# Kernel optimization log

Hardware: AMD Instinct MI355X
Metric: run time of the kernel (lower is better)

The kernel has to match this reference:

```python
import jax, jax.numpy as jnp
import numpy as np

M_BITS = 8   # mantissa bits (m in BlockQuantize)
E_BITS = 8   # exponent bits (e)
GROUP_D = 64 # column-group width from group_shapes [64,64]


def bfp_quantize_2d(W, d=GROUP_D, m=M_BITS, e=E_BITS):
    """Faithful vectorized BlockQuantize2D with calculate_bias=True.
    Groups = 64-wide column blocks spanning all rows (tensor.reshape(-1,d)[start::new_width])."""
    a, b = W.shape
    nw = b // d
    # [nw, a*d]: each row is one quantization group
    blocks = W.reshape(a, nw, d).transpose(1, 0, 2).reshape(nw, a * d)
    maxv = jnp.max(jnp.abs(blocks), axis=1, keepdims=True)
    bias = 2.0 ** e - jnp.log2(maxv) + jnp.log2(2.0 - 2.0 ** (-m + 1)) - 1.0
    max_exp = 2.0 ** e - 1.0 - bias
    max_val = 2.0 ** max_exp * (1.0 + (1.0 - 2.0 ** (-m - 1)))
    sign = jnp.sign(blocks)
    absx = jnp.clip(jnp.abs(blocks), -max_val, max_val)  # lower bound negative -> no-op, as in source
    exponent = jnp.floor(jnp.log2(absx + 1e-40))
    mantissa = absx / 2.0 ** exponent                    # in [1, 2)
    group_exp = jnp.max(exponent, axis=1, keepdims=True)
    group_exp = jnp.where(group_exp + bias < 1.0, -bias, group_exp)
    # shiftTruncateInBinaryForm
    factor = 2 ** (m - 1)                                # 128
    sm = (mantissa * factor).astype(jnp.int32)           # [128, 256)
    shift = jnp.clip((group_exp - exponent).astype(jnp.int32), 0, 31)
    shifted = jnp.right_shift(sm, shift)
    safe = jnp.maximum(shifted, 1)
    bitlen = (jnp.floor(jnp.log2(safe.astype(jnp.float32))) + 1.0).astype(jnp.int32)
    mask = jnp.where(bitlen > 8, jnp.left_shift(jnp.int32(255), bitlen - 8), jnp.int32(255))
    trunc = jnp.bitwise_and(shifted, mask).astype(jnp.float32) / factor
    q = sign * trunc * 2.0 ** group_exp
    return q.reshape(nw, a, d).transpose(1, 0, 2).reshape(a, b)


def apply_rope(t, cos, sin):
    """t: [b,s,h,hd]; complex rotation on (even, odd) pairs as in apply_rotary_emb."""
    tr = t.reshape(*t.shape[:-1], -1, 2)
    te, to = tr[..., 0], tr[..., 1]
    c = cos[None, :, None, :]
    s = sin[None, :, None, :]
    oe = te * c - to * s
    oo = te * s + to * c
    return jnp.stack([oe, oo], axis=-1).reshape(t.shape)


def setup_inputs() -> dict:
    key = jax.random.key(0)
    k = jax.random.split(key, 5)
    dim, n_heads, n_kv, hd = 4096, 32, 8, 128
    b, s = 1, 2048
    x = jax.random.normal(k[0], (b, s, dim), jnp.float32)
    wq = jax.random.normal(k[1], (n_heads * hd, dim), jnp.float32) * 0.02
    wk = jax.random.normal(k[2], (n_kv * hd, dim), jnp.float32) * 0.02
    wv = jax.random.normal(k[3], (n_kv * hd, dim), jnp.float32) * 0.02
    wo = jax.random.normal(k[4], (dim, n_heads * hd), jnp.float32) * 0.02
    inv_freq = 1.0 / (10000.0 ** (jnp.arange(0, hd, 2, dtype=jnp.float32) / hd))
    ang = jnp.outer(jnp.arange(s, dtype=jnp.float32), inv_freq)  # [s, hd/2]
    return {"x": x, "wq": wq, "wk": wk, "wv": wv, "wo": wo,
            "freqs_cos": jnp.cos(ang), "freqs_sin": jnp.sin(ang)}


def reference(x, wq, wk, wv, wo, freqs_cos, freqs_sin):
    b, s, dim = x.shape
    n_heads, n_kv, hd = 32, 8, 128
    n_rep = n_heads // n_kv
    # block-floating-point quantization of projection weights (per-64-column groups)
    wq_q = bfp_quantize_2d(wq)
    wk_q = bfp_quantize_2d(wk)
    wv_q = bfp_quantize_2d(wv)
    wo_q = bfp_quantize_2d(wo)
    q = jnp.einsum('bsd,od->bso', x, wq_q).reshape(b, s, n_heads, hd)
    kk = jnp.einsum('bsd,od->bso', x, wk_q).reshape(b, s, n_kv, hd)
    v = jnp.einsum('bsd,od->bso', x, wv_q).reshape(b, s, n_kv, hd)
    q = apply_rope(q, freqs_cos, freqs_sin)
    kk = apply_rope(kk, freqs_cos, freqs_sin)
    # repeat_kv: GQA expand kv heads by n_rep
    kk = jnp.repeat(kk, n_rep, axis=2)  # [b,s,n_heads,hd]
    v = jnp.repeat(v, n_rep, axis=2)
    scores = jnp.einsum('bshd,bthd->bhst', q, kk) / jnp.sqrt(jnp.float32(hd))
    causal = jnp.triu(jnp.full((s, s), -jnp.inf, dtype=scores.dtype), k=1)
    probs = jax.nn.softmax(scores + causal, axis=-1)
    out = jnp.einsum('bhst,bthd->bshd', probs, v).reshape(b, s, n_heads * hd)
    return jnp.einsum('bso,do->bsd', out, wo_q)
```

## Files before the change

### kernel.cpp

```cpp
#include <hip/hip_runtime.h>
#include <hip/hip_bf16.h>

typedef __hip_bfloat16 hbf16;
typedef __bf16 bf16x8 __attribute__((ext_vector_type(8)));
typedef float f32x4 __attribute__((ext_vector_type(4)));

#define MFMA16(a, b, c) __builtin_amdgcn_mfma_f32_16x16x32_bf16((a), (b), (c), 0, 0, 0)

#define ASYNC16(ldsaddr, gaddr)                                                        \
  __builtin_amdgcn_global_load_lds(                                                    \
      (__attribute__((address_space(1))) void*)(void*)(gaddr),                         \
      (__attribute__((address_space(3))) void*)(ldsaddr), 16, 0, 0)

static __device__ __forceinline__ float fexp2(float x) {
#if __has_builtin(__builtin_amdgcn_exp2f)
  return __builtin_amdgcn_exp2f(x);
#else
  return exp2f(x);
#endif
}

__global__ void init_gmax_kernel(unsigned int* g) { g[threadIdx.x] = 0u; }

__global__ void quant_max_kernel(const float* __restrict__ wq, const float* __restrict__ wk,
                                 const float* __restrict__ wv, const float* __restrict__ wo,
                                 unsigned int* __restrict__ gmax) {
  const int my = blockIdx.y;
  const float* W;
  int slotBase, rowsPerSplit;
  if (my == 0) { W = wq; slotBase = 0;   rowsPerSplit = 512; }
  else if (my == 1) { W = wk; slotBase = 64;  rowsPerSplit = 128; }
  else if (my == 2) { W = wv; slotBase = 128; rowsPerSplit = 128; }
  else { W = wo; slotBase = 192; rowsPerSplit = 512; }
  const int tid = threadIdx.x;
  const int group = blockIdx.x & 63;
  const int split = blockIdx.x >> 6;
  const int c4 = (tid & 15) * 4;
  const int rs = tid >> 4;
  const float* base = W + (size_t)(split * rowsPerSplit) * 4096 + group * 64 + c4;
  float m = 0.f;
  for (int r = rs; r < rowsPerSplit; r += 16) {
    float4 v = *(const float4*)(base + (size_t)r * 4096);
    m = fmaxf(m, fmaxf(fmaxf(fabsf(v.x), fabsf(v.y)), fmaxf(fabsf(v.z), fabsf(v.w))));
  }
  for (int d = 1; d < 64; d <<= 1) m = fmaxf(m, __shfl_xor(m, d, 64));
  __shared__ float wm_[4];
  if ((tid & 63) == 0) wm_[tid >> 6] = m;
  __syncthreads();
  if (tid == 0) {
    m = fmaxf(fmaxf(wm_[0], wm_[1]), fmaxf(wm_[2], wm_[3]));
    atomicMax(gmax + slotBase + group, __float_as_uint(m));
  }
}

__device__ __forceinline__ void quant_body(const float* __restrict__ W, hbf16* __restrict__ Wq,
                                           const unsigned int* __restrict__ gmax, int slotBase,
                                           int n4) {
  const int stride = gridDim.x * 256;
  for (int idx = blockIdx.x * 256 + threadIdx.x; idx < n4; idx += stride) {
    int group = (idx & 1023) >> 4;
    unsigned int mb = gmax[slotBase + group];
    int gex = (int)((mb >> 23) & 255) - 127;
    float s = __uint_as_float((unsigned)(134 - gex) << 23);
    float inv = __uint_as_float((unsigned)(120 + gex) << 23);
    float4 w = *(const float4*)(W + (size_t)idx * 4);
    hbf16 t[4];
    t[0] = __float2bfloat16(truncf(w.x * s) * inv);
    t[1] = __float2bfloat16(truncf(w.y * s) * inv);
    t[2] = __float2bfloat16(truncf(w.z * s) * inv);
    t[3] = __float2bfloat16(truncf(w.w * s) * inv);
    *(uint2*)(Wq + (size_t)idx * 4) = *(uint2*)t;
  }
}

__global__ void quant_apply_qkv_kernel(const float* __restrict__ wq, const float* __restrict__ wk,
                                       const float* __restrict__ wv, hbf16* __restrict__ Wq,
                                       const unsigned int* __restrict__ gmax) {
  const int my = blockIdx.y;
  if (my == 0) quant_body(wq, Wq, gmax, 0, 4096 * 4096 / 4);
  else if (my == 1) quant_body(wk, Wq + (size_t)4096 * 4096, gmax, 64, 1024 * 4096 / 4);
  else quant_body(wv, Wq + (size_t)5120 * 4096, gmax, 128, 1024 * 4096 / 4);
}

__global__ void quant_apply_kernel(const float* __restrict__ W, hbf16* __restrict__ Wq,
                                   const unsigned int* __restrict__ gmax, int slotBase, int n4) {
  quant_body(W, Wq, gmax, slotBase, n4);
}

__global__ void cvt_bf16_kernel(const float* __restrict__ X, hbf16* __restrict__ Y, int n4) {
  const int stride = gridDim.x * 256;
  for (int idx = blockIdx.x * 256 + threadIdx.x; idx < n4; idx += stride) {
    float4 v = *(const float4*)(X + (size_t)idx * 4);
    hbf16 t[4] = {__float2bfloat16(v.x), __float2bfloat16(v.y),
                  __float2bfloat16(v.z), __float2bfloat16(v.w)};
    *(uint2*)(Y + (size_t)idx * 4) = *(uint2*)t;
  }
}

__global__ void rope_kernel(const float* __restrict__ In, const float* __restrict__ Cs,
                            const float* __restrict__ Sn, hbf16* __restrict__ Out,
                            int shift, int rowStride, float scale) {
  int i = blockIdx.x * 256 + threadIdx.x;
  int ppr = 1 << shift;
  if (i >= 2048 * ppr) return;
  int s = i >> shift;
  int p = i & (ppr - 1);
  int t = p & 63;
  float2 q = *(const float2*)(In + (size_t)s * rowStride + p * 2);
  float c = Cs[s * 64 + t] * scale, sn = Sn[s * 64 + t] * scale;
  hbf16 o[2] = {__float2bfloat16(q.x * c - q.y * sn), __float2bfloat16(q.x * sn + q.y * c)};
  *(unsigned int*)(Out + (size_t)s * ppr * 2 + p * 2) = *(unsigned int*)o;
}

__global__ void transpose_v_kernel(const float* __restrict__ QKV, hbf16* __restrict__ Vt) {
  __shared__ float tile[64][65];
  const int g = blockIdx.x, sb = blockIdx.y, db = blockIdx.z;
  const int tid = threadIdx.x;
  const int c = tid & 63;
  for (int r = tid >> 6; r < 64; r += 4)
    tile[r][c] = QKV[(size_t)(sb * 64 + r) * 6144 + 5120 + g * 128 + db * 64 + c];
  __syncthreads();
  for (int r = tid >> 6; r < 64; r += 4)
    Vt[(size_t)g * 262144 + (size_t)(db * 64 + r) * 2048 + sb * 64 + c] =
        __float2bfloat16(tile[c][r]);
}

__global__ __launch_bounds__(256) void gemm_bt_kernel(const hbf16* __restrict__ A,
                                                      const hbf16* __restrict__ Bt,
                                                      float* __restrict__ C, int N) {
  constexpr int K = 4096;
  __shared__ __align__(16) hbf16 sA[128 * 64];
  __shared__ __align__(16) hbf16 sB[128 * 64];
  const int tid = threadIdx.x;
  const int wave = tid >> 6, lane = tid & 63;
  const int l15 = lane & 15, quad = lane >> 4;
  const int bm = blockIdx.x, bn = blockIdx.y;
  const int wm = (wave >> 1) * 64, wn = (wave & 1) * 64;

  const char* Ab = (const char*)(A + (size_t)bm * 128 * K);
  const char* Bb = (const char*)(Bt + (size_t)bn * 128 * K);
  char* sAb = (char*)sA;
  char* sBb = (char*)sB;

  f32x4 acc[4][4];
#pragma unroll
  for (int i = 0; i < 4; ++i)
#pragma unroll
    for (int n = 0; n < 4; ++n) acc[i][n] = (f32x4){0.f, 0.f, 0.f, 0.f};

  for (int kk = 0; kk < K; kk += 64) {
#pragma unroll
    for (int r = 0; r < 4; ++r) {
      int f = r * 4096 + tid * 16;
      int row = f >> 7;
      int lc = ((f >> 4) & 7) ^ (row & 7);
      ASYNC16(sAb + f, Ab + (size_t)row * (K * 2) + kk * 2 + lc * 16);
      ASYNC16(sBb + f, Bb + (size_t)row * (K * 2) + kk * 2 + lc * 16);
    }
    __syncthreads();
#pragma unroll
    for (int kc = 0; kc < 2; ++kc) {
      bf16x8 af[4], bg[4];
#pragma unroll
      for (int i = 0; i < 4; ++i)
        af[i] = *(const bf16x8*)(sAb + (wm + i * 16 + l15) * 128 +
                                 (((kc << 2) | quad) ^ (l15 & 7)) * 16);
#pragma unroll
      for (int n = 0; n < 4; ++n)
        bg[n] = *(const bf16x8*)(sBb + (wn + n * 16 + l15) * 128 +
                                 (((kc << 2) | quad) ^ (l15 & 7)) * 16);
#pragma unroll
      for (int i = 0; i < 4; ++i)
#pragma unroll
        for (int n = 0; n < 4; ++n) acc[i][n] = MFMA16(af[i], bg[n], acc[i][n]);
    }
    __syncthreads();
  }
#pragma unroll
  for (int i = 0; i < 4; ++i) {
    int row = bm * 128 + wm + i * 16 + quad * 4;
#pragma unroll
    for (int n = 0; n < 4; ++n) {
      float* cp = C + (size_t)row * N + bn * 128 + wn + n * 16 + l15;
#pragma unroll
      for (int r = 0; r < 4; ++r) cp[(size_t)r * N] = acc[i][n][r];
    }
  }
}

__global__ __launch_bounds__(256, 4) void attn_kernel(const hbf16* __restrict__ Q,
                                                      const hbf16* __restrict__ Kr,
                                                      const hbf16* __restrict__ Vt,
                                                      hbf16* __restrict__ O) {
  __shared__ __align__(16) hbf16 sK[64 * 128];
  __shared__ __align__(16) hbf16 sV[128 * 64];
  const int tid = threadIdx.x;
  const int wave = tid >> 6, lane = tid & 63;
  const int l15 = lane & 15, quad = lane >> 4;
  const int bid = blockIdx.x;
  const int h = bid >> 5;
  const int qb = (31 - (bid & 31) + 8 * ((bid >> 8) & 3)) & 31;
  const int g = h >> 2;
  const int qrow0 = qb * 64 + wave * 16;
  const int qrow = qrow0 + l15;

  bf16x8 qf[4];
  {
    const hbf16* qp = Q + (size_t)qrow * 4096 + h * 128 + quad * 8;
#pragma unroll
    for (int kc = 0; kc < 4; ++kc) qf[kc] = *(const bf16x8*)(qp + kc * 32);
  }
  f32x4 of[8];
#pragma unroll
  for (int nf = 0; nf < 8; ++nf) of[nf] = (f32x4){0.f, 0.f, 0.f, 0.f};
  float m_i = -1e30f, l_i = 0.f;

  const char* Kb = (const char*)Kr + (size_t)g * 256;
  const char* Vb = (const char*)Vt + (size_t)g * 524288;
  char* sKb = (char*)sK;
  char* sVb = (char*)sV;

  const int nkb = qb + 1;
  for (int kb = 0; kb < nkb; ++kb) {
#pragma unroll
    for (int r = 0; r < 4; ++r) {
      int f = r * 4096 + tid * 16;
      {
        int row = f >> 8;
        int lc = ((f >> 4) & 15) ^ (row & 15);
        ASYNC16(sKb + f, Kb + (size_t)(kb * 64 + row) * 2048 + lc * 16);
      }
      {
        int row = f >> 7;
        int lc = ((f >> 4) & 7) ^ (row & 7);
        ASYNC16(sVb + f, Vb + (size_t)row * 4096 + kb * 128 + lc * 16);
      }
    }
    __syncthreads();

    f32x4 sacc[4];
#pragma unroll
    for (int n = 0; n < 4; ++n) sacc[n] = (f32x4){0.f, 0.f, 0.f, 0.f};
#pragma unroll
    for (int n = 0; n < 4; ++n)
#pragma unroll
      for (int kc = 0; kc < 4; ++kc) {
        bf16x8 kf = *(const bf16x8*)(sKb + (n * 16 + l15) * 256 +
                                     (((kc << 2) | quad) ^ l15) * 16);
        sacc[n] = MFMA16(kf, qf[kc], sacc[n]);
      }

    float p[4][4];
    float mx = -1e30f;
    if (kb == qb) {
      const int key0 = kb * 64 + quad * 4;
#pragma unroll
      for (int n = 0; n < 4; ++n)
#pragma unroll
        for (int r = 0; r < 4; ++r) {
          float s = sacc[n][r];
          s = (key0 + n * 16 + r > qrow) ? -1e30f : s;
          p[n][r] = s;
          mx = fmaxf(mx, s);
        }
    } else {
#pragma unroll
      for (int n = 0; n < 4; ++n)
#pragma unroll
        for (int r = 0; r < 4; ++r) {
          p[n][r] = sacc[n][r];
          mx = fmaxf(mx, sacc[n][r]);
        }
    }
    mx = fmaxf(mx, __shfl_xor(mx, 16, 64));
    mx = fmaxf(mx, __shfl_xor(mx, 32, 64));
    float mnew = fmaxf(m_i, mx);
    float alpha = fexp2(m_i - mnew);
    m_i = mnew;
    float sum = 0.f;
#pragma unroll
    for (int n = 0; n < 4; ++n)
#pragma unroll
      for (int r = 0; r < 4; ++r) {
        p[n][r] = fexp2(p[n][r] - mnew);
        sum += p[n][r];
      }
    sum += __shfl_xor(sum, 16, 64);
    sum += __shfl_xor(sum, 32, 64);
    l_i = l_i * alpha + sum;
#pragma unroll
    for (int nf = 0; nf < 8; ++nf)
#pragma unroll
      for (int r = 0; r < 4; ++r) of[nf][r] *= alpha;

    unsigned pk[8];
#pragma unroll
    for (int n = 0; n < 4; ++n)
#pragma unroll
      for (int h2 = 0; h2 < 2; ++h2) {
        hbf16 t2[2] = {__float2bfloat16(p[n][2 * h2]), __float2bfloat16(p[n][2 * h2 + 1])};
        pk[n * 2 + h2] = *(unsigned*)t2;
      }

    const int sa = ((quad & 1) << 5) + l15;
    const int sb2 = sa + 16;
#pragma unroll
    for (int kc = 0; kc < 2; ++kc) {
      unsigned a0 = __shfl((int)pk[kc * 4 + 0], sa, 64);
      unsigned a1 = __shfl((int)pk[kc * 4 + 1], sa, 64);
      unsigned a2 = __shfl((int)pk[kc * 4 + 2], sa, 64);
      unsigned a3 = __shfl((int)pk[kc * 4 + 3], sa, 64);
      unsigned b0 = __shfl((int)pk[kc * 4 + 0], sb2, 64);
      unsigned b1 = __shfl((int)pk[kc * 4 + 1], sb2, 64);
      unsigned b2 = __shfl((int)pk[kc * 4 + 2], sb2, 64);
      unsigned b3 = __shfl((int)pk[kc * 4 + 3], sb2, 64);
      union {
        unsigned u[4];
        bf16x8 v;
      } pf;
      pf.u[0] = (quad < 2) ? a0 : a2;
      pf.u[1] = (quad < 2) ? a1 : a3;
      pf.u[2] = (quad < 2) ? b0 : b2;
      pf.u[3] = (quad < 2) ? b1 : b3;
#pragma unroll
      for (int nf = 0; nf < 8; ++nf) {
        bf16x8 vf = *(const bf16x8*)(sVb + (nf * 16 + l15) * 128 +
                                     (((kc << 2) | quad) ^ (l15 & 7)) * 16);
        of[nf] = MFMA16(vf, pf.v, of[nf]);
      }
    }
    __syncthreads();
  }

  const float invl = 1.f / l_i;
#pragma unroll
  for (int nf = 0; nf < 8; ++nf) {
    hbf16 t4[4];
#pragma unroll
    for (int r = 0; r < 4; ++r) t4[r] = __float2bfloat16(of[nf][r] * invl);
    *(uint2*)(O + (size_t)qrow * 4096 + h * 128 + nf * 16 + quad * 4) = *(uint2*)t4;
  }
}

extern "C" void kernel_launch(void* const* d_in, const int* in_sizes, int n_in,
                              void* d_out, int out_size, void* d_ws, size_t ws_size,
                              hipStream_t stream) {
  const float* x = (const float*)d_in[0];
  const float* wq = (const float*)d_in[1];
  const float* wk = (const float*)d_in[2];
  const float* wv = (const float*)d_in[3];
  const float* wo = (const float*)d_in[4];
  const float* fc = (const float*)d_in[5];
  const float* fs = (const float*)d_in[6];
  float* out = (float*)d_out;

  char* w = (char*)d_ws;
  size_t off = 0;
  auto alloc = [&](size_t bytes) -> char* {
    char* p = w + off;
    off += (bytes + 255) & ~(size_t)255;
    return p;
  };
  unsigned int* gmax = (unsigned int*)alloc(1024);
  hbf16* xb = (hbf16*)alloc((size_t)2048 * 4096 * 2);
  hbf16* wqkv = (hbf16*)alloc((size_t)6144 * 4096 * 2);
  float* qkv = (float*)alloc((size_t)2048 * 6144 * 4);
  hbf16* qrope = (hbf16*)alloc((size_t)2048 * 4096 * 2);
  hbf16* krope = (hbf16*)alloc((size_t)2048 * 1024 * 2);
  hbf16* vt = (hbf16*)alloc((size_t)8 * 128 * 2048 * 2);
  hbf16* woq = wqkv;
  hbf16* attno = (hbf16*)qkv;

  const float kSc = 0.12753139668280277f;

  init_gmax_kernel<<<1, 256, 0, stream>>>(gmax);
  quant_max_kernel<<<dim3(512, 4), 256, 0, stream>>>(wq, wk, wv, wo, gmax);
  quant_apply_qkv_kernel<<<dim3(2048, 3), 256, 0, stream>>>(wq, wk, wv, wqkv, gmax);
  cvt_bf16_kernel<<<2048, 256, 0, stream>>>(x, xb, 2048 * 4096 / 4);
  gemm_bt_kernel<<<dim3(16, 48), 256, 0, stream>>>(xb, wqkv, qkv, 6144);
  quant_apply_kernel<<<2048, 256, 0, stream>>>(wo, woq, gmax, 192, 4096 * 4096 / 4);
  rope_kernel<<<16384, 256, 0, stream>>>(qkv, fc, fs, qrope, 11, 6144, kSc);
  rope_kernel<<<4096, 256, 0, stream>>>(qkv + 4096, fc, fs, krope, 9, 6144, 1.0f);
  transpose_v_kernel<<<dim3(8, 32, 2), 256, 0, stream>>>(qkv, vt);
  attn_kernel<<<1024, 256, 0, stream>>>(qrope, krope, vt, attno);
  gemm_bt_kernel<<<dim3(16, 32), 256, 0, stream>>>(attno, woq, out, 4096);
  (void)in_sizes; (void)n_in; (void)out_size; (void)ws_size;
}
```

Measured before the change: 588.3 us.

## Fuse prep/postproc kernels, drop atomic max init, retile GEMM N tiles

Replaces the atomicMax group-max reduction with per-split partial maxima, so the init kernel is no longer needed and the max is reduced when it is read. Merges weight quantization with the x-to-bf16 conversion into one prep kernel, and merges wo quantization, both RoPE passes and the V transpose into one postproc kernel, cutting launch count. The GEMM is templated on the N tile, using 96 columns for QKV (1024 blocks) and 64 for the output projection (1024 blocks) to fill more CUs, at the cost of less reuse per block. The quantization scale is now loaded once per thread, which relies on the grid stride keeping each thread in the same group.

```diff
diff --git a/kernel.cpp b/kernel.cpp
--- a/kernel.cpp
+++ b/kernel.cpp
@@ -20,11 +20,9 @@
 #endif
 }
 
-__global__ void init_gmax_kernel(unsigned int* g) { g[threadIdx.x] = 0u; }
-
 __global__ void quant_max_kernel(const float* __restrict__ wq, const float* __restrict__ wk,
                                  const float* __restrict__ wv, const float* __restrict__ wo,
-                                 unsigned int* __restrict__ gmax) {
+                                 unsigned int* __restrict__ gmaxs) {
   const int my = blockIdx.y;
   const float* W;
   int slotBase, rowsPerSplit;
@@ -49,20 +47,24 @@
   __syncthreads();
   if (tid == 0) {
     m = fmaxf(fmaxf(wm_[0], wm_[1]), fmaxf(wm_[2], wm_[3]));
-    atomicMax(gmax + slotBase + group, __float_as_uint(m));
+    gmaxs[(slotBase + group) * 8 + split] = __float_as_uint(m);
   }
 }
 
 __device__ __forceinline__ void quant_body(const float* __restrict__ W, hbf16* __restrict__ Wq,
-                                           const unsigned int* __restrict__ gmax, int slotBase,
-                                           int n4) {
-  const int stride = gridDim.x * 256;
-  for (int idx = blockIdx.x * 256 + threadIdx.x; idx < n4; idx += stride) {
-    int group = (idx & 1023) >> 4;
-    unsigned int mb = gmax[slotBase + group];
-    int gex = (int)((mb >> 23) & 255) - 127;
-    float s = __uint_as_float((unsigned)(134 - gex) << 23);
-    float inv = __uint_as_float((unsigned)(120 + gex) << 23);
+                                           const unsigned int* __restrict__ gmaxs, int slotBase,
+                                           int n4, int block0, int nblocks) {
+  const int stride = nblocks * 256;
+  const int idx0 = block0 * 256 + (int)threadIdx.x;
+  if (idx0 >= n4) return;
+  const int slot = slotBase + ((idx0 & 1023) >> 4);
+  unsigned int mb = 0;
+#pragma unroll
+  for (int sp = 0; sp < 8; ++sp) mb = max(mb, gmaxs[slot * 8 + sp]);
+  int gex = (int)((mb >> 23) & 255) - 127;
+  float s = __uint_as_float((unsigned)(134 - gex) << 23);
+  float inv = __uint_as_float((unsigned)(120 + gex) << 23);
+  for (int idx = idx0; idx < n4; idx += stride) {
     float4 w = *(const float4*)(W + (size_t)idx * 4);
     hbf16 t[4];
     t[0] = __float2bfloat16(truncf(w.x * s) * inv);
@@ -73,80 +75,89 @@
   }
 }
 
-__global__ void quant_apply_qkv_kernel(const float* __restrict__ wq, const float* __restrict__ wk,
-                                       const float* __restrict__ wv, hbf16* __restrict__ Wq,
-                                       const unsigned int* __restrict__ gmax) {
+__global__ void prep_kernel(const float* __restrict__ wq, const float* __restrict__ wk,
+                            const float* __restrict__ wv, const float* __restrict__ x,
+                            hbf16* __restrict__ Wqkv, hbf16* __restrict__ xb,
+                            const unsigned int* __restrict__ gmaxs) {
   const int my = blockIdx.y;
-  if (my == 0) quant_body(wq, Wq, gmax, 0, 4096 * 4096 / 4);
-  else if (my == 1) quant_body(wk, Wq + (size_t)4096 * 4096, gmax, 64, 1024 * 4096 / 4);
-  else quant_body(wv, Wq + (size_t)5120 * 4096, gmax, 128, 1024 * 4096 / 4);
-}
-
-__global__ void quant_apply_kernel(const float* __restrict__ W, hbf16* __restrict__ Wq,
-                                   const unsigned int* __restrict__ gmax, int slotBase, int n4) {
-  quant_body(W, Wq, gmax, slotBase, n4);
-}
-
-__global__ void cvt_bf16_kernel(const float* __restrict__ X, hbf16* __restrict__ Y, int n4) {
-  const int stride = gridDim.x * 256;
-  for (int idx = blockIdx.x * 256 + threadIdx.x; idx < n4; idx += stride) {
-    float4 v = *(const float4*)(X + (size_t)idx * 4);
-    hbf16 t[4] = {__float2bfloat16(v.x), __float2bfloat16(v.y),
-                  __float2bfloat16(v.z), __float2bfloat16(v.w)};
-    *(uint2*)(Y + (size_t)idx * 4) = *(uint2*)t;
-  }
-}
-
-__global__ void rope_kernel(const float* __restrict__ In, const float* __restrict__ Cs,
-                            const float* __restrict__ Sn, hbf16* __restrict__ Out,
-                            int shift, int rowStride, float scale) {
-  int i = blockIdx.x * 256 + threadIdx.x;
-  int ppr = 1 << shift;
-  if (i >= 2048 * ppr) return;
-  int s = i >> shift;
-  int p = i & (ppr - 1);
-  int t = p & 63;
-  float2 q = *(const float2*)(In + (size_t)s * rowStride + p * 2);
-  float c = Cs[s * 64 + t] * scale, sn = Sn[s * 64 + t] * scale;
-  hbf16 o[2] = {__float2bfloat16(q.x * c - q.y * sn), __float2bfloat16(q.x * sn + q.y * c)};
-  *(unsigned int*)(Out + (size_t)s * ppr * 2 + p * 2) = *(unsigned int*)o;
-}
-
-__global__ void transpose_v_kernel(const float* __restrict__ QKV, hbf16* __restrict__ Vt) {
+  if (my == 0) {
+    quant_body(wq, Wqkv, gmaxs, 0, 4096 * 4096 / 4, blockIdx.x, gridDim.x);
+  } else if (my == 1) {
+    quant_body(wk, Wqkv + (size_t)4096 * 4096, gmaxs, 64, 1024 * 4096 / 4, blockIdx.x, gridDim.x);
+  } else if (my == 2) {
+    quant_body(wv, Wqkv + (size_t)5120 * 4096, gmaxs, 128, 1024 * 4096 / 4, blockIdx.x, gridDim.x);
+  } else {
+    const int stride = gridDim.x * 256;
+    for (int idx = blockIdx.x * 256 + threadIdx.x; idx < 2048 * 4096 / 4; idx += stride) {
+      float4 v = *(const float4*)(x + (size_t)idx * 4);
+      hbf16 t[4] = {__float2bfloat16(v.x), __float2bfloat16(v.y),
+                    __float2bfloat16(v.z), __float2bfloat16(v.w)};
+      *(uint2*)(xb + (size_t)idx * 4) = *(uint2*)t;
+    }
+  }
+}
+
+__global__ void postproc_kernel(const float* __restrict__ wo, hbf16* __restrict__ woq,
+                                const unsigned int* __restrict__ gmaxs,
+                                const float* __restrict__ qkv, const float* __restrict__ Cs,
+                                const float* __restrict__ Sn, hbf16* __restrict__ qrope,
+                                hbf16* __restrict__ krope, hbf16* __restrict__ Vt, float qscale) {
   __shared__ float tile[64][65];
-  const int g = blockIdx.x, sb = blockIdx.y, db = blockIdx.z;
+  const int bid = blockIdx.x;
   const int tid = threadIdx.x;
-  const int c = tid & 63;
-  for (int r = tid >> 6; r < 64; r += 4)
-    tile[r][c] = QKV[(size_t)(sb * 64 + r) * 6144 + 5120 + g * 128 + db * 64 + c];
-  __syncthreads();
-  for (int r = tid >> 6; r < 64; r += 4)
-    Vt[(size_t)g * 262144 + (size_t)(db * 64 + r) * 2048 + sb * 64 + c] =
-        __float2bfloat16(tile[c][r]);
-}
-
+  if (bid < 2048) {
+    quant_body(wo, woq, gmaxs, 192, 4096 * 4096 / 4, bid, 2048);
+  } else if (bid < 18432) {
+    int i = (bid - 2048) * 256 + tid;
+    int s = i >> 11, p = i & 2047, t = p & 63;
+    float2 q = *(const float2*)(qkv + (size_t)s * 6144 + p * 2);
+    float c = Cs[s * 64 + t] * qscale, sn = Sn[s * 64 + t] * qscale;
+    hbf16 o[2] = {__float2bfloat16(q.x * c - q.y * sn), __float2bfloat16(q.x * sn + q.y * c)};
+    *(unsigned int*)(qrope + (size_t)s * 4096 + p * 2) = *(unsigned int*)o;
+  } else if (bid < 22528) {
+    int i = (bid - 18432) * 256 + tid;
+    int s = i >> 9, p = i & 511, t = p & 63;
+    float2 q = *(const float2*)(qkv + (size_t)s * 6144 + 4096 + p * 2);
+    float c = Cs[s * 64 + t], sn = Sn[s * 64 + t];
+    hbf16 o[2] = {__float2bfloat16(q.x * c - q.y * sn), __float2bfloat16(q.x * sn + q.y * c)};
+    *(unsigned int*)(krope + (size_t)s * 1024 + p * 2) = *(unsigned int*)o;
+  } else {
+    int id = bid - 22528;
+    int g = id & 7, sb = (id >> 3) & 31, db = id >> 8;
+    int c = tid & 63;
+    for (int r = tid >> 6; r < 64; r += 4)
+      tile[r][c] = qkv[(size_t)(sb * 64 + r) * 6144 + 5120 + g * 128 + db * 64 + c];
+    __syncthreads();
+    for (int r = tid >> 6; r < 64; r += 4)
+      Vt[(size_t)g * 262144 + (size_t)(db * 64 + r) * 2048 + sb * 64 + c] =
+          __float2bfloat16(tile[c][r]);
+  }
+}
+
+template <int BN>
 __global__ __launch_bounds__(256) void gemm_bt_kernel(const hbf16* __restrict__ A,
                                                       const hbf16* __restrict__ Bt,
                                                       float* __restrict__ C, int N) {
   constexpr int K = 4096;
+  constexpr int NF = BN / 32;
   __shared__ __align__(16) hbf16 sA[128 * 64];
-  __shared__ __align__(16) hbf16 sB[128 * 64];
+  __shared__ __align__(16) hbf16 sB[BN * 64];
   const int tid = threadIdx.x;
   const int wave = tid >> 6, lane = tid & 63;
   const int l15 = lane & 15, quad = lane >> 4;
   const int bm = blockIdx.x, bn = blockIdx.y;
-  const int wm = (wave >> 1) * 64, wn = (wave & 1) * 64;
+  const int wm = (wave >> 1) * 64, wn = (wave & 1) * (BN / 2);
 
   const char* Ab = (const char*)(A + (size_t)bm * 128 * K);
-  const char* Bb = (const char*)(Bt + (size_t)bn * 128 * K);
+  const char* Bb = (const char*)(Bt + (size_t)bn * BN * K);
   char* sAb = (char*)sA;
   char* sBb = (char*)sB;
 
-  f32x4 acc[4][4];
+  f32x4 acc[4][NF];
 #pragma unroll
   for (int i = 0; i < 4; ++i)
 #pragma unroll
-    for (int n = 0; n < 4; ++n) acc[i][n] = (f32x4){0.f, 0.f, 0.f, 0.f};
+    for (int n = 0; n < NF; ++n) acc[i][n] = (f32x4){0.f, 0.f, 0.f, 0.f};
 
   for (int kk = 0; kk < K; kk += 64) {
 #pragma unroll
@@ -155,24 +166,30 @@
       int row = f >> 7;
       int lc = ((f >> 4) & 7) ^ (row & 7);
       ASYNC16(sAb + f, Ab + (size_t)row * (K * 2) + kk * 2 + lc * 16);
+    }
+#pragma unroll
+    for (int r = 0; r < NF; ++r) {
+      int f = r * 4096 + tid * 16;
+      int row = f >> 7;
+      int lc = ((f >> 4) & 7) ^ (row & 7);
       ASYNC16(sBb + f, Bb + (size_t)row * (K * 2) + kk * 2 + lc * 16);
     }
     __syncthreads();
 #pragma unroll
     for (int kc = 0; kc < 2; ++kc) {
-      bf16x8 af[4], bg[4];
+      bf16x8 af[4], bg[NF];
 #pragma unroll
       for (int i = 0; i < 4; ++i)
         af[i] = *(const bf16x8*)(sAb + (wm + i * 16 + l15) * 128 +
                                  (((kc << 2) | quad) ^ (l15 & 7)) * 16);
 #pragma unroll
-      for (int n = 0; n < 4; ++n)
+      for (int n = 0; n < NF; ++n)
         bg[n] = *(const bf16x8*)(sBb + (wn + n * 16 + l15) * 128 +
                                  (((kc << 2) | quad) ^ (l15 & 7)) * 16);
 #pragma unroll
       for (int i = 0; i < 4; ++i)
 #pragma unroll
-        for (int n = 0; n < 4; ++n) acc[i][n] = MFMA16(af[i], bg[n], acc[i][n]);
+        for (int n = 0; n < NF; ++n) acc[i][n] = MFMA16(af[i], bg[n], acc[i][n]);
     }
     __syncthreads();
   }
@@ -180,8 +197,8 @@
   for (int i = 0; i < 4; ++i) {
     int row = bm * 128 + wm + i * 16 + quad * 4;
 #pragma unroll
-    for (int n = 0; n < 4; ++n) {
-      float* cp = C + (size_t)row * N + bn * 128 + wn + n * 16 + l15;
+    for (int n = 0; n < NF; ++n) {
+      float* cp = C + (size_t)row * N + bn * BN + wn + n * 16 + l15;
 #pragma unroll
       for (int r = 0; r < 4; ++r) cp[(size_t)r * N] = acc[i][n][r];
     }
@@ -361,7 +378,7 @@
     off += (bytes + 255) & ~(size_t)255;
     return p;
   };
-  unsigned int* gmax = (unsigned int*)alloc(1024);
+  unsigned int* gmaxs = (unsigned int*)alloc(256 * 8 * 4);
   hbf16* xb = (hbf16*)alloc((size_t)2048 * 4096 * 2);
   hbf16* wqkv = (hbf16*)alloc((size_t)6144 * 4096 * 2);
   float* qkv = (float*)alloc((size_t)2048 * 6144 * 4);
@@ -373,16 +390,11 @@
 
   const float kSc = 0.12753139668280277f;
 
-  init_gmax_kernel<<<1, 256, 0, stream>>>(gmax);
-  quant_max_kernel<<<dim3(512, 4), 256, 0, stream>>>(wq, wk, wv, wo, gmax);
-  quant_apply_qkv_kernel<<<dim3(2048, 3), 256, 0, stream>>>(wq, wk, wv, wqkv, gmax);
-  cvt_bf16_kernel<<<2048, 256, 0, stream>>>(x, xb, 2048 * 4096 / 4);
-  gemm_bt_kernel<<<dim3(16, 48), 256, 0, stream>>>(xb, wqkv, qkv, 6144);
-  quant_apply_kernel<<<2048, 256, 0, stream>>>(wo, woq, gmax, 192, 4096 * 4096 / 4);
-  rope_kernel<<<16384, 256, 0, stream>>>(qkv, fc, fs, qrope, 11, 6144, kSc);
-  rope_kernel<<<4096, 256, 0, stream>>>(qkv + 4096, fc, fs, krope, 9, 6144, 1.0f);
-  transpose_v_kernel<<<dim3(8, 32, 2), 256, 0, stream>>>(qkv, vt);
+  quant_max_kernel<<<dim3(512, 4), 256, 0, stream>>>(wq, wk, wv, wo, gmaxs);
+  prep_kernel<<<dim3(2048, 4), 256, 0, stream>>>(wq, wk, wv, x, wqkv, xb, gmaxs);
+  gemm_bt_kernel<96><<<dim3(16, 64), 256, 0, stream>>>(xb, wqkv, qkv, 6144);
+  postproc_kernel<<<23040, 256, 0, stream>>>(wo, woq, gmaxs, qkv, fc, fs, qrope, krope, vt, kSc);
   attn_kernel<<<1024, 256, 0, stream>>>(qrope, krope, vt, attno);
-  gemm_bt_kernel<<<dim3(16, 32), 256, 0, stream>>>(attno, woq, out, 4096);
+  gemm_bt_kernel<64><<<dim3(16, 64), 256, 0, stream>>>(attno, woq, out, 4096);
   (void)in_sizes; (void)n_in; (void)out_size; (void)ws_size;
 }
```

Measured after the change: 571.4 us. -2.9%, faster.
